# Performance work log

Measured on AMD Instinct MI355X. Metric: run time of the kernel, lower is better.

## Reference

```python
import jax, jax.numpy as jnp
import numpy as np

NUM_NODES = 50000
NUM_RELS = 47        # 2*23 + 1 after enrich()
EMB_DIM = 1600
WEIGHTS_SIZE = 16
NUM_CLASSES = 50
BASES = 40
NUM_EDGES = 1600000


def setup_inputs() -> dict:
    key = jax.random.key(0)
    ks = jax.random.split(key, 8)
    return {
        "node_embeddings": jax.random.normal(ks[0], (NUM_NODES, EMB_DIM), jnp.float32),
        "comps1": jax.random.normal(ks[1], (NUM_RELS, BASES), jnp.float32),
        "bases1": jax.random.normal(ks[2], (BASES, EMB_DIM, WEIGHTS_SIZE), jnp.float32) * 0.05,
        "comps2": jax.random.normal(ks[3], (NUM_RELS, BASES), jnp.float32),
        "bases2": jax.random.normal(ks[4], (BASES, WEIGHTS_SIZE, NUM_CLASSES), jnp.float32) * 0.05,
        "bias1": jnp.zeros((WEIGHTS_SIZE,), jnp.float32),
        "bias2": jnp.zeros((NUM_CLASSES,), jnp.float32),
        "rows": jax.random.randint(ks[5], (NUM_EDGES,), 0, NUM_NODES, jnp.int32),
        "cols": jax.random.randint(ks[6], (NUM_EDGES,), 0, NUM_RELS * NUM_NODES, jnp.int32),
    }


def _spmm(rows, cols, vals, h_rel):
    # hor_graph @ h_rel : h_rel is (R*N, d); out[n] = sum_e vals[e] * h_rel[cols[e]]
    msgs = vals[:, None] * h_rel[cols]              # (E, d)
    return jax.ops.segment_sum(msgs, rows, num_segments=NUM_NODES)


def reference(node_embeddings, comps1, bases1, comps2, bases2, bias1, bias2, rows, cols):
    R, N = NUM_RELS, NUM_NODES
    # normalization: 1 / row-sums of vertical adjacency == 1 / counts per hor column
    cnt = jax.ops.segment_sum(jnp.ones_like(cols, jnp.float32), cols, num_segments=R * N)
    vals = 1.0 / cnt[cols]                          # (E,)

    # layer 1: basis-decomposed per-relation transform
    w1 = jnp.einsum('rb,bio->rio', comps1, bases1)  # (R, emb, ws)
    h = jnp.einsum('ni,rio->rno', node_embeddings, w1)  # (R, N, ws)
    h = h.reshape(R * N, WEIGHTS_SIZE)
    h = _spmm(rows, cols, vals, h)                  # (N, ws)
    h = jax.nn.relu(h + bias1)

    # layer 2
    w2 = jnp.einsum('rb,bio->rio', comps2, bases2)  # (R, ws, C)
    h = jnp.einsum('ni,rio->rno', h, w2)            # (R, N, C)
    h = h.reshape(R * N, NUM_CLASSES)
    h = _spmm(rows, cols, vals, h)                  # (N, C)
    return h + bias2
```

## Files before the change

### kernel.cpp

```cpp
#include <hip/hip_runtime.h>
#include <hip/hip_bf16.h>

#define NN 50000
#define RR 47
#define ED 1600
#define WS 16
#define NC 50
#define NB 40
#define NE 1600000
#define WJ (RR*WS)
#define WJP 768

typedef unsigned short ushort_t;
typedef short s16x8 __attribute__((ext_vector_type(8)));
typedef float f32x4 __attribute__((ext_vector_type(4)));

__device__ __forceinline__ ushort_t f2bf(float f) {
    __hip_bfloat16 h = __float2bfloat16(f);
    ushort_t u;
    __builtin_memcpy(&u, &h, 2);
    return u;
}
__device__ __forceinline__ float bf2f(ushort_t u) {
    unsigned v = ((unsigned)u) << 16;
    float f;
    __builtin_memcpy(&f, &v, 4);
    return f;
}

__device__ __forceinline__ void async_copy16(const ushort_t* g, ushort_t* l) {
    __builtin_amdgcn_global_load_lds(
        (const __attribute__((address_space(1))) unsigned int*)g,
        (__attribute__((address_space(3))) unsigned int*)l,
        16, 0, 0);
}

__global__ void cast_kernel(const float* __restrict__ X, ushort_t* __restrict__ A) {
    int idx = blockIdx.x * blockDim.x + threadIdx.x;
    if (idx >= (NN * ED) / 4) return;
    float4 v = ((const float4*)X)[idx];
    ushort_t* p = &A[idx * 4];
    p[0] = f2bf(v.x); p[1] = f2bf(v.y); p[2] = f2bf(v.z); p[3] = f2bf(v.w);
}

__global__ void count_kernel(const int* __restrict__ cols, float* __restrict__ cnt) {
    int e = blockIdx.x * blockDim.x + threadIdx.x;
    if (e < NE) atomicAdd(&cnt[cols[e]], 1.0f);
}

__global__ void wbigbt_kernel(const float* __restrict__ comps1, const float* __restrict__ bases1,
                              ushort_t* __restrict__ WbigB) {
    int idx = blockIdx.x * blockDim.x + threadIdx.x;
    if (idx >= WJP * ED) return;
    int j = idx / ED;
    int i = idx - j * ED;
    float s = 0.f;
    if (j < WJ) {
        int r = j >> 4;
        int o = j & 15;
#pragma unroll
        for (int b = 0; b < NB; ++b)
            s += comps1[r * NB + b] * bases1[(b * ED + i) * WS + o];
    }
    WbigB[idx] = f2bf(s);
}

__global__ __launch_bounds__(256) void mfma_gemm_kernel(const ushort_t* __restrict__ A,
                                                        const ushort_t* __restrict__ B,
                                                        ushort_t* __restrict__ C) {
    __shared__ ushort_t Abuf[128 * 32];
    __shared__ ushort_t Bbuf[128 * 32];

    const int t = threadIdx.x;
    const int lane = t & 63;
    const int wave = t >> 6;
    const int m0 = blockIdx.x * 128;
    const int n0 = blockIdx.y * 128;
    const int wm = (wave & 1) * 64;
    const int wn = (wave >> 1) * 64;

    const int arow0 = t >> 2,        akp0 = (t & 3) * 8;
    const int arow1 = (t + 256) >> 2, akp1 = ((t + 256) & 3) * 8;
    int gm0 = m0 + arow0; if (gm0 >= NN) gm0 = NN - 1;
    int gm1 = m0 + arow1; if (gm1 >= NN) gm1 = NN - 1;
    const ushort_t* ap0 = &A[(size_t)gm0 * ED + akp0];
    const ushort_t* ap1 = &A[(size_t)gm1 * ED + akp1];
    const ushort_t* bp0 = &B[(size_t)(n0 + arow0) * ED + akp0];
    const ushort_t* bp1 = &B[(size_t)(n0 + arow1) * ED + akp1];

    f32x4 acc[4][4];
#pragma unroll
    for (int i = 0; i < 4; ++i)
#pragma unroll
        for (int j = 0; j < 4; ++j) acc[i][j] = (f32x4){0.f, 0.f, 0.f, 0.f};

    const int frow = lane & 15;
    const int fk = (lane >> 4) * 8;

    for (int k0 = 0; k0 < ED; k0 += 32) {
        async_copy16(ap0 + k0, &Abuf[t * 8]);
        async_copy16(ap1 + k0, &Abuf[(t + 256) * 8]);
        async_copy16(bp0 + k0, &Bbuf[t * 8]);
        async_copy16(bp1 + k0, &Bbuf[(t + 256) * 8]);
        __syncthreads();

        s16x8 af[4], bf[4];
#pragma unroll
        for (int mt = 0; mt < 4; ++mt)
            af[mt] = *(const s16x8*)&Abuf[(wm + mt * 16 + frow) * 32 + fk];
#pragma unroll
        for (int nt = 0; nt < 4; ++nt)
            bf[nt] = *(const s16x8*)&Bbuf[(wn + nt * 16 + frow) * 32 + fk];
#pragma unroll
        for (int mt = 0; mt < 4; ++mt)
#pragma unroll
            for (int nt = 0; nt < 4; ++nt)
                acc[mt][nt] = __builtin_amdgcn_mfma_f32_16x16x32_bf16(af[mt], bf[nt], acc[mt][nt], 0, 0, 0);
        __syncthreads();
    }

    const int cm = (lane >> 4) * 4;
    const int cn = lane & 15;
#pragma unroll
    for (int mt = 0; mt < 4; ++mt) {
#pragma unroll
        for (int i = 0; i < 4; ++i) {
            int gm = m0 + wm + mt * 16 + cm + i;
            if (gm >= NN) continue;
#pragma unroll
            for (int nt = 0; nt < 4; ++nt) {
                int gn = n0 + wn + nt * 16 + cn;
                if (gn < WJ) C[(size_t)gm * WJ + gn] = f2bf(acc[mt][nt][i]);
            }
        }
    }
}

__global__ void spmm1_kernel(const int* __restrict__ rows, const int* __restrict__ cols,
                             const float* __restrict__ cnt, const ushort_t* __restrict__ hrel,
                             float* __restrict__ h1) {
    int tid = blockIdx.x * blockDim.x + threadIdx.x;
    int e = tid >> 4;
    if (e >= NE) return;
    int o = tid & 15;
    int col = cols[e];
    int row = rows[e];
    float v = 1.0f / cnt[col];
    int r = col / NN;
    int n = col - r * NN;
    float x = bf2f(hrel[(size_t)n * WJ + r * WS + o]);
    atomicAdd(&h1[row * WS + o], v * x);
}

__global__ void relu_kernel(float* __restrict__ h1, const float* __restrict__ bias1) {
    int idx = blockIdx.x * blockDim.x + threadIdx.x;
    if (idx >= NN * WS) return;
    float v = h1[idx] + bias1[idx & 15];
    h1[idx] = v > 0.f ? v : 0.f;
}

__global__ void w2_kernel(const float* __restrict__ comps2, const float* __restrict__ bases2,
                          float* __restrict__ w2) {
    int idx = blockIdx.x * blockDim.x + threadIdx.x;
    if (idx >= RR * WS * NC) return;
    int r = idx / (WS * NC);
    int rem = idx - r * (WS * NC);
    float s = 0.f;
#pragma unroll
    for (int b = 0; b < NB; ++b)
        s += comps2[r * NB + b] * bases2[b * (WS * NC) + rem];
    w2[idx] = s;
}

__global__ void initout_kernel(float* __restrict__ out, const float* __restrict__ bias2) {
    int idx = blockIdx.x * blockDim.x + threadIdx.x;
    if (idx >= NN * NC) return;
    out[idx] = bias2[idx % NC];
}

__global__ void spmm2_kernel(const int* __restrict__ rows, const int* __restrict__ cols,
                             const float* __restrict__ cnt, const float* __restrict__ h1,
                             const float* __restrict__ w2, float* __restrict__ out) {
    int tid = blockIdx.x * blockDim.x + threadIdx.x;
    int e = tid >> 6;
    int c = tid & 63;
    if (e >= NE || c >= NC) return;
    int col = cols[e];
    int row = rows[e];
    float v = 1.0f / cnt[col];
    int r = col / NN;
    int n = col - r * NN;
    const float* hp = &h1[n * WS];
    const float* wp = &w2[r * (WS * NC) + c];
    float s = 0.f;
#pragma unroll
    for (int o = 0; o < WS; ++o) s += hp[o] * wp[o * NC];
    atomicAdd(&out[row * NC + c], v * s);
}

extern "C" void kernel_launch(void* const* d_in, const int* in_sizes, int n_in,
                              void* d_out, int out_size, void* d_ws, size_t ws_size,
                              hipStream_t stream) {
    const float* X      = (const float*)d_in[0];
    const float* comps1 = (const float*)d_in[1];
    const float* bases1 = (const float*)d_in[2];
    const float* comps2 = (const float*)d_in[3];
    const float* bases2 = (const float*)d_in[4];
    const float* bias1  = (const float*)d_in[5];
    const float* bias2  = (const float*)d_in[6];
    const int*   rows   = (const int*)d_in[7];
    const int*   cols   = (const int*)d_in[8];
    float* out = (float*)d_out;

    char* ws = (char*)d_ws;
    float*    cnt   = (float*)   (ws + 0);
    ushort_t* Abf   = (ushort_t*)(ws + 9400064);
    ushort_t* WbigB = (ushort_t*)(ws + 169400064);
    ushort_t* hrel  = (ushort_t*)(ws + 171857664);
    float*    h1    = (float*)   (ws + 247057664);
    float*    w2    = (float*)   (ws + 250257664);

    hipMemsetAsync(cnt, 0, (size_t)RR * NN * 4, stream);
    hipMemsetAsync(h1, 0, (size_t)NN * WS * 4, stream);

    cast_kernel<<<(NN * ED / 4 + 255) / 256, 256, 0, stream>>>(X, Abf);
    count_kernel<<<(NE + 255) / 256, 256, 0, stream>>>(cols, cnt);
    wbigbt_kernel<<<(WJP * ED + 255) / 256, 256, 0, stream>>>(comps1, bases1, WbigB);

    dim3 ggrid((NN + 127) / 128, WJP / 128);
    mfma_gemm_kernel<<<ggrid, 256, 0, stream>>>(Abf, WbigB, hrel);

    spmm1_kernel<<<(NE * 16) / 256, 256, 0, stream>>>(rows, cols, cnt, hrel, h1);
    relu_kernel<<<(NN * WS + 255) / 256, 256, 0, stream>>>(h1, bias1);
    w2_kernel<<<(RR * WS * NC + 255) / 256, 256, 0, stream>>>(comps2, bases2, w2);
    initout_kernel<<<(NN * NC + 255) / 256, 256, 0, stream>>>(out, bias2);
    spmm2_kernel<<<(NE * 64) / 256, 256, 0, stream>>>(rows, cols, cnt, h1, w2, out);
}
```

Measured before the change: 1.368 ms.

## Reorder layer-2 as aggregate-then-transform with per-relation scatter and dense GEMM

Layer 2 used to compute each edge's 16x50 transform inside the scatter and issue 50 atomics per edge. It now scatters normalized h1 rows into a per-node, per-relation buffer G of size N x (R*16), then runs one tiled fp32 GEMM against the stacked W2 and adds the bias. This cuts atomics per edge from 50 to 16 and removes the redundant per-edge matmul. In exchange it adds a 150MB memset plus a GEMM that reads G, and G reuses the bf16 A workspace.

```diff
diff --git a/kernel.cpp b/kernel.cpp
--- a/kernel.cpp
+++ b/kernel.cpp
@@ -159,43 +159,95 @@
     h1[idx] = v > 0.f ? v : 0.f;
 }
 
-__global__ void w2_kernel(const float* __restrict__ comps2, const float* __restrict__ bases2,
-                          float* __restrict__ w2) {
-    int idx = blockIdx.x * blockDim.x + threadIdx.x;
-    if (idx >= RR * WS * NC) return;
-    int r = idx / (WS * NC);
-    int rem = idx - r * (WS * NC);
+__global__ void w2p_kernel(const float* __restrict__ comps2, const float* __restrict__ bases2,
+                           float* __restrict__ w2p) {
+    int idx = blockIdx.x * blockDim.x + threadIdx.x;
+    if (idx >= WJ * 64) return;
+    int k = idx >> 6;
+    int c = idx & 63;
     float s = 0.f;
-#pragma unroll
-    for (int b = 0; b < NB; ++b)
-        s += comps2[r * NB + b] * bases2[b * (WS * NC) + rem];
-    w2[idx] = s;
-}
-
-__global__ void initout_kernel(float* __restrict__ out, const float* __restrict__ bias2) {
-    int idx = blockIdx.x * blockDim.x + threadIdx.x;
-    if (idx >= NN * NC) return;
-    out[idx] = bias2[idx % NC];
-}
-
-__global__ void spmm2_kernel(const int* __restrict__ rows, const int* __restrict__ cols,
-                             const float* __restrict__ cnt, const float* __restrict__ h1,
-                             const float* __restrict__ w2, float* __restrict__ out) {
+    if (c < NC) {
+        int r = k >> 4;
+        int o = k & 15;
+#pragma unroll
+        for (int b = 0; b < NB; ++b)
+            s += comps2[r * NB + b] * bases2[(b * WS + o) * NC + c];
+    }
+    w2p[idx] = s;
+}
+
+__global__ void agg_kernel(const int* __restrict__ rows, const int* __restrict__ cols,
+                           const float* __restrict__ cnt, const float* __restrict__ h1,
+                           float* __restrict__ G) {
     int tid = blockIdx.x * blockDim.x + threadIdx.x;
-    int e = tid >> 6;
-    int c = tid & 63;
-    if (e >= NE || c >= NC) return;
+    int e = tid >> 4;
+    if (e >= NE) return;
+    int o = tid & 15;
     int col = cols[e];
     int row = rows[e];
     float v = 1.0f / cnt[col];
     int r = col / NN;
     int n = col - r * NN;
-    const float* hp = &h1[n * WS];
-    const float* wp = &w2[r * (WS * NC) + c];
-    float s = 0.f;
-#pragma unroll
-    for (int o = 0; o < WS; ++o) s += hp[o] * wp[o * NC];
-    atomicAdd(&out[row * NC + c], v * s);
+    float x = h1[n * WS + o];
+    atomicAdd(&G[(size_t)row * WJ + r * WS + o], v * x);
+}
+
+__global__ __launch_bounds__(256) void gemm2_kernel(const float* __restrict__ G,
+                                                    const float* __restrict__ w2p,
+                                                    const float* __restrict__ bias2,
+                                                    float* __restrict__ out) {
+    __shared__ float As[16][64];
+    __shared__ float Bs[16][64 + 4];
+
+    int t = threadIdx.x;
+    int m0 = blockIdx.x * 64;
+    int tx = t & 15, ty = t >> 4;
+
+    float acc[4][4] = {};
+
+    int arow = t >> 2, ak = (t & 3) * 4;
+    int bk = t >> 4, bn = (t & 15) * 4;
+
+    for (int k0 = 0; k0 < WJ; k0 += 16) {
+        {
+            int gm = m0 + arow;
+            float4 av = make_float4(0.f, 0.f, 0.f, 0.f);
+            if (gm < NN) av = *(const float4*)&G[(size_t)gm * WJ + k0 + ak];
+            As[ak + 0][arow] = av.x;
+            As[ak + 1][arow] = av.y;
+            As[ak + 2][arow] = av.z;
+            As[ak + 3][arow] = av.w;
+        }
+        {
+            float4 bv = *(const float4*)&w2p[(k0 + bk) * 64 + bn];
+            *(float4*)&Bs[bk][bn] = bv;
+        }
+        __syncthreads();
+#pragma unroll
+        for (int k = 0; k < 16; ++k) {
+            float4 a = *(const float4*)&As[k][ty * 4];
+            float4 b = *(const float4*)&Bs[k][tx * 4];
+            float av[4] = {a.x, a.y, a.z, a.w};
+            float bv[4] = {b.x, b.y, b.z, b.w};
+#pragma unroll
+            for (int i = 0; i < 4; ++i)
+#pragma unroll
+                for (int j = 0; j < 4; ++j)
+                    acc[i][j] += av[i] * bv[j];
+        }
+        __syncthreads();
+    }
+
+#pragma unroll
+    for (int i = 0; i < 4; ++i) {
+        int gm = m0 + ty * 4 + i;
+        if (gm >= NN) break;
+#pragma unroll
+        for (int j = 0; j < 4; ++j) {
+            int gn = tx * 4 + j;
+            if (gn < NC) out[gm * NC + gn] = acc[i][j] + bias2[gn];
+        }
+    }
 }
 
 extern "C" void kernel_launch(void* const* d_in, const int* in_sizes, int n_in,
@@ -215,10 +267,11 @@
     char* ws = (char*)d_ws;
     float*    cnt   = (float*)   (ws + 0);
     ushort_t* Abf   = (ushort_t*)(ws + 9400064);
+    float*    G     = (float*)   (ws + 9400064);
     ushort_t* WbigB = (ushort_t*)(ws + 169400064);
     ushort_t* hrel  = (ushort_t*)(ws + 171857664);
     float*    h1    = (float*)   (ws + 247057664);
-    float*    w2    = (float*)   (ws + 250257664);
+    float*    w2p   = (float*)   (ws + 250257664);
 
     hipMemsetAsync(cnt, 0, (size_t)RR * NN * 4, stream);
     hipMemsetAsync(h1, 0, (size_t)NN * WS * 4, stream);
@@ -232,7 +285,10 @@
 
     spmm1_kernel<<<(NE * 16) / 256, 256, 0, stream>>>(rows, cols, cnt, hrel, h1);
     relu_kernel<<<(NN * WS + 255) / 256, 256, 0, stream>>>(h1, bias1);
-    w2_kernel<<<(RR * WS * NC + 255) / 256, 256, 0, stream>>>(comps2, bases2, w2);
-    initout_kernel<<<(NN * NC + 255) / 256, 256, 0, stream>>>(out, bias2);
-    spmm2_kernel<<<(NE * 64) / 256, 256, 0, stream>>>(rows, cols, cnt, h1, w2, out);
-}
+    w2p_kernel<<<(WJ * 64 + 255) / 256, 256, 0, stream>>>(comps2, bases2, w2p);
+
+    hipMemsetAsync(G, 0, (size_t)NN * WJ * 4, stream);
+    agg_kernel<<<(NE * 16) / 256, 256, 0, stream>>>(rows, cols, cnt, h1, G);
+
+    gemm2_kernel<<<(NN + 63) / 64, 256, 0, stream>>>(G, w2p, bias2, out);
+}
```

New measurement: 1.102 ms. 19.5% less time.
